# Optimization experiments

Measured on AMD Instinct MI355X. Metric: run time of the kernel, lower is better.

## Reference

```python
import jax, jax.numpy as jnp
import numpy as np

N = 100000
E = 1600000
DIM_IN, DIM_H, DIM_OUT = 48, 48, 48


def gcn_conv(x, edge_index, W, b):
    # PyG GCNConv: add self-loops, symmetric normalization D^-1/2 (A+I) D^-1/2, linear first.
    n = x.shape[0]
    loop = jnp.arange(n, dtype=edge_index.dtype)
    row = jnp.concatenate([edge_index[0], loop])  # sources
    col = jnp.concatenate([edge_index[1], loop])  # targets
    deg = jax.ops.segment_sum(jnp.ones_like(col, dtype=x.dtype), col, num_segments=n)
    dinv = jnp.where(deg > 0, jax.lax.rsqrt(jnp.maximum(deg, 1e-12)), 0.0)
    norm = dinv[row] * dinv[col]  # [E+N]
    h = x @ W  # [N, out]
    msg = h[row] * norm[:, None]  # gather + scale, [E+N, out]
    out = jax.ops.segment_sum(msg, col, num_segments=n)  # scatter-add
    return out + b


def setup_inputs() -> dict:
    key = jax.random.key(0)
    ks = jax.random.split(key, 8)
    x = jax.random.normal(ks[0], (N, DIM_IN), dtype=jnp.float32)
    edge_index = jax.random.randint(ks[1], (2, E), 0, N, dtype=jnp.int64)
    s1 = 1.0 / np.sqrt(DIM_IN)
    s2 = 1.0 / np.sqrt(DIM_H)
    s3 = 1.0 / np.sqrt(DIM_OUT)
    W1 = jax.random.uniform(ks[2], (DIM_IN, DIM_H), jnp.float32, -s1, s1)
    b1 = jnp.zeros((DIM_H,), jnp.float32)
    W2 = jax.random.uniform(ks[3], (DIM_H, DIM_OUT), jnp.float32, -s2, s2)
    b2 = jnp.zeros((DIM_OUT,), jnp.float32)
    Wlin = jax.random.uniform(ks[4], (DIM_OUT, 2), jnp.float32, -s3, s3)
    blin = jax.random.uniform(ks[5], (2,), jnp.float32, -s3, s3)
    return {"x": x, "edge_index": edge_index, "W1": W1, "b1": b1, "W2": W2, "b2": b2, "Wlin": Wlin, "blin": blin}


def reference(x, edge_index, W1, b1, W2, b2, Wlin, blin):
    h = gcn_conv(x, edge_index, W1, b1)
    h = jax.nn.leaky_relu(h, negative_slope=0.01)
    h = gcn_conv(h, edge_index, W2, b2)
    # global_add_pool with all-zero batch ids -> sum over all nodes, [1, DIM_OUT]
    g = jnp.sum(h, axis=0, keepdims=True)
    # dropout is identity in eval mode
    return g @ Wlin + blin  # [1, 2]
```

## Files before the change

### kernel.cpp

```cpp
#include <hip/hip_runtime.h>
#include <hip/hip_bf16.h>
#include <hip/hip_fp8.h>

#define DIM 48
#define HS8 48
#define BKN 256
#define BSH 8
#define CAP 5248
#define NB1MAX 400
#define EPT 12
#define GNPB 64
#define GTPN 3

typedef float v2f __attribute__((ext_vector_type(2)));

__device__ inline unsigned pack_fp8x4(float a, float b, float c, float d) {
#if __has_builtin(__builtin_amdgcn_cvt_pk_fp8_f32)
    int w = __builtin_amdgcn_cvt_pk_fp8_f32(a, b, 0, false);
    w = __builtin_amdgcn_cvt_pk_fp8_f32(c, d, w, true);
    return (unsigned)w;
#else
    __hip_fp8_e4m3 qa(a), qb(b), qc(c), qd(d);
    return (unsigned)qa.__x | ((unsigned)qb.__x << 8) |
           ((unsigned)qc.__x << 16) | ((unsigned)qd.__x << 24);
#endif
}

__device__ inline void acc_fp8x4(unsigned w, float* acc) {
#if __has_builtin(__builtin_amdgcn_cvt_pk_f32_fp8)
    v2f lo = __builtin_amdgcn_cvt_pk_f32_fp8((int)w, false);
    v2f hi = __builtin_amdgcn_cvt_pk_f32_fp8((int)w, true);
    acc[0] += lo[0]; acc[1] += lo[1]; acc[2] += hi[0]; acc[3] += hi[1];
#else
    __hip_fp8_e4m3 q0, q1, q2, q3;
    q0.__x = (unsigned char)(w & 0xff);
    q1.__x = (unsigned char)((w >> 8) & 0xff);
    q2.__x = (unsigned char)((w >> 16) & 0xff);
    q3.__x = (unsigned char)(w >> 24);
    acc[0] += (float)q0; acc[1] += (float)q1;
    acc[2] += (float)q2; acc[3] += (float)q3;
#endif
}

__device__ inline void acc_fp8x16(uint4 v, float* acc) {
    acc_fp8x4(v.x, acc + 0);
    acc_fp8x4(v.y, acc + 4);
    acc_fp8x4(v.z, acc + 8);
    acc_fp8x4(v.w, acc + 12);
}

__global__ void k_zero(int* __restrict__ cntc, int* __restrict__ cntr,
                       float* __restrict__ g, int nb1) {
    int i = blockIdx.x * blockDim.x + threadIdx.x;
    if (i < nb1) { cntc[i] = 0; cntr[i] = 0; }
    if (i < 64) g[i] = 0.0f;
}

__global__ __launch_bounds__(256) void k_part(
    const int* __restrict__ row, const int* __restrict__ col,
    int* __restrict__ cntc, int* __restrict__ cntr,
    unsigned* __restrict__ partc, unsigned* __restrict__ partr, int E, int nb1) {
    __shared__ int hc[NB1MAX], hr[NB1MAX];
    __shared__ int bc_[NB1MAX], br_[NB1MAX];
    int t = threadIdx.x;
    int lo = blockIdx.x * (256 * EPT);
    int hi = min(lo + 256 * EPT, E);
    int ec[EPT], er[EPT];
    int m = 0;
    for (int e = lo + t; e < hi; e += 256) { ec[m] = col[e]; er[m] = row[e]; ++m; }
    for (int i = t; i < nb1; i += 256) { hc[i] = 0; hr[i] = 0; }
    __syncthreads();
    for (int k = 0; k < m; ++k) {
        atomicAdd(&hc[ec[k] >> BSH], 1);
        atomicAdd(&hr[er[k] >> BSH], 1);
    }
    __syncthreads();
    for (int i = t; i < nb1; i += 256) {
        bc_[i] = hc[i] ? atomicAdd(&cntc[i], hc[i]) : 0;
        br_[i] = hr[i] ? atomicAdd(&cntr[i], hr[i]) : 0;
        hc[i] = 0; hr[i] = 0;
    }
    __syncthreads();
    for (int k = 0; k < m; ++k) {
        int c = ec[k], r = er[k];
        int b1 = c >> BSH;
        unsigned p1 = (unsigned)(bc_[b1] + atomicAdd(&hc[b1], 1));
        if (p1 < (unsigned)CAP)
            partc[(size_t)b1 * CAP + p1] = ((unsigned)(c & (BKN - 1)) << 24) | (unsigned)r;
        int b2 = r >> BSH;
        unsigned p2 = (unsigned)(br_[b2] + atomicAdd(&hr[b2], 1));
        if (p2 < (unsigned)CAP)
            partr[(size_t)b2 * CAP + p2] = ((unsigned)(r & (BKN - 1)) << 24) | (unsigned)c;
    }
}

__global__ __launch_bounds__(256) void k_sortp(
    const unsigned* __restrict__ partc, const int* __restrict__ cntc,
    int* __restrict__ nodpk, float* __restrict__ dinv,
    int* __restrict__ srcs, int N, int nb1) {
    __shared__ int cnt[BKN];
    __shared__ int cur[BKN];
    __shared__ int sc[256];
    __shared__ int outb[CAP];
    int b = blockIdx.x, t = threadIdx.x;
    int nlo = b << BSH;
    int nE = min(cntc[b], CAP);
    const unsigned* pp = partc + (size_t)b * CAP;
    cnt[t] = 0;
    __syncthreads();
    for (int e = t; e < nE; e += 256)
        atomicAdd(&cnt[pp[e] >> 24], 1);
    __syncthreads();
    int v = cnt[t];
    sc[t] = v;
    __syncthreads();
    for (int off = 1; off < 256; off <<= 1) {
        int u = (t >= off) ? sc[t - off] : 0;
        __syncthreads();
        sc[t] += u;
        __syncthreads();
    }
    int ex = (t == 0) ? 0 : sc[t - 1];
    if (nlo + t < N) {
        nodpk[nlo + t] = ex | (v << 16);
        dinv[nlo + t] = 1.0f / sqrtf((float)(v + 1));
    }
    cur[t] = ex;
    __syncthreads();
    for (int e = t; e < nE; e += 256) {
        unsigned p = pp[e];
        int s = atomicAdd(&cur[p >> 24], 1);
        outb[s] = (int)(p & 0xffffffu);
    }
    __syncthreads();
    int* sb = srcs + (size_t)b * CAP;
    for (int i2 = t; i2 < nE; i2 += 256) sb[i2] = outb[i2];
}

__global__ __launch_bounds__(256) void k_wsum(
    const unsigned* __restrict__ partr, const int* __restrict__ cntr,
    const float* __restrict__ dinv, float* __restrict__ wfin, int N, int nb1) {
    __shared__ float ws[BKN];
    int b = blockIdx.x, t = threadIdx.x;
    ws[t] = 0.0f;
    __syncthreads();
    int nE = min(cntr[b], CAP);
    const unsigned* pp = partr + (size_t)b * CAP;
    for (int e = t; e < nE; e += 256) {
        unsigned p = pp[e];
        atomicAdd(&ws[p >> 24], dinv[p & 0xffffffu]);
    }
    __syncthreads();
    int j = (b << BSH) + t;
    if (j < N) {
        float dj = dinv[j];
        wfin[j] = (ws[t] + dj) * dj;
    }
}

__global__ void k_mm_scale(const float* __restrict__ in, const float* __restrict__ W,
                           const float* __restrict__ dinv,
                           unsigned char* __restrict__ hs8, int n) {
    __shared__ float Ws[DIM * DIM];
    for (int i = threadIdx.x; i < DIM * DIM; i += blockDim.x) Ws[i] = W[i];
    __syncthreads();
    int node = blockIdx.x * blockDim.x + threadIdx.x;
    if (node >= n) return;
    float xr[DIM];
    const float4* xp = (const float4*)(in + (size_t)node * DIM);
    #pragma unroll
    for (int j = 0; j < DIM / 4; ++j) {
        float4 v = xp[j];
        xr[j * 4 + 0] = v.x; xr[j * 4 + 1] = v.y;
        xr[j * 4 + 2] = v.z; xr[j * 4 + 3] = v.w;
    }
    float o[DIM];
    #pragma unroll
    for (int f = 0; f < DIM; ++f) o[f] = 0.0f;
    for (int k = 0; k < DIM; ++k) {
        float xv = xr[k];
        #pragma unroll
        for (int f = 0; f < DIM; ++f) o[f] = fmaf(xv, Ws[k * DIM + f], o[f]);
    }
    float d = dinv[node];
    uint4* hp = (uint4*)(hs8 + (size_t)node * HS8);
    #pragma unroll
    for (int q = 0; q < 3; ++q) {
        uint4 v;
        v.x = pack_fp8x4(o[q*16+ 0]*d, o[q*16+ 1]*d, o[q*16+ 2]*d, o[q*16+ 3]*d);
        v.y = pack_fp8x4(o[q*16+ 4]*d, o[q*16+ 5]*d, o[q*16+ 6]*d, o[q*16+ 7]*d);
        v.z = pack_fp8x4(o[q*16+ 8]*d, o[q*16+ 9]*d, o[q*16+10]*d, o[q*16+11]*d);
        v.w = pack_fp8x4(o[q*16+12]*d, o[q*16+13]*d, o[q*16+14]*d, o[q*16+15]*d);
        hp[q] = v;
    }
}

__global__ __launch_bounds__(GNPB * GTPN) void k_gather1f(
    const unsigned char* __restrict__ hs8,
    const int* __restrict__ nodpk, const int* __restrict__ srcs,
    const float* __restrict__ dinv, const float* __restrict__ wfin,
    const float* __restrict__ bias, float* __restrict__ g, int n) {
    __shared__ float gsum[DIM];
    int t = threadIdx.x;
    if (t < DIM) gsum[t] = 0.0f;
    __syncthreads();
    int local = t / GTPN;
    int c = t - local * GTPN;
    int i = blockIdx.x * GNPB + local;
    bool valid = (i < n);
    float ov[16];
    if (valid) {
        int pk = nodpk[i];
        int start = (i >> BSH) * CAP + (pk & 0xffff);
        int end = start + (pk >> 16);
        float d = dinv[i];
        float w = wfin[i];
        const unsigned char* hb = hs8 + (size_t)c * 16;
        float acc[16];
        #pragma unroll
        for (int k = 0; k < 16; ++k) acc[k] = 0.0f;
        uint4 sv = *(const uint4*)(hb + (size_t)i * HS8);
        acc_fp8x16(sv, acc);
        for (int j = start; j < end; ++j) {
            uint4 v = *(const uint4*)(hb + (size_t)srcs[j] * HS8);
            acc_fp8x16(v, acc);
        }
        #pragma unroll
        for (int k = 0; k < 16; ++k) {
            float vv = acc[k] * d + bias[c * 16 + k];
            vv = (vv >= 0.0f) ? vv : 0.01f * vv;
            ov[k] = vv * w;
        }
    }
    if (valid) {
        #pragma unroll
        for (int k = 0; k < 16; ++k) atomicAdd(&gsum[c * 16 + k], ov[k]);
    }
    __syncthreads();
    if (t < DIM) atomicAdd(&g[t], gsum[t]);
}

__global__ void k_final2(const float* __restrict__ g, const float* __restrict__ W2,
                         const float* __restrict__ b2, const float* __restrict__ Wlin,
                         const float* __restrict__ blin, float* __restrict__ out, int n) {
    __shared__ float gp[DIM];
    int t = threadIdx.x;
    if (t < DIM) {
        float s = (float)n * b2[t];
        for (int q = 0; q < DIM; ++q) s += g[q] * W2[q * DIM + t];
        gp[t] = s;
    }
    __syncthreads();
    if (t < 2) {
        float s = blin[t];
        for (int f = 0; f < DIM; ++f) s += gp[f] * Wlin[f * 2 + t];
        out[t] = s;
    }
}

static inline char* alignup(char* p, size_t a) {
    return (char*)(((uintptr_t)p + a - 1) & ~(uintptr_t)(a - 1));
}

extern "C" void kernel_launch(void* const* d_in, const int* in_sizes, int n_in,
                              void* d_out, int out_size, void* d_ws, size_t ws_size,
                              hipStream_t stream) {
    const float* x    = (const float*)d_in[0];
    const int*   ei   = (const int*)d_in[1];
    const float* W1   = (const float*)d_in[2];
    const float* b1   = (const float*)d_in[3];
    const float* W2   = (const float*)d_in[4];
    const float* b2   = (const float*)d_in[5];
    const float* Wlin = (const float*)d_in[6];
    const float* blin = (const float*)d_in[7];
    float* out = (float*)d_out;

    int N = in_sizes[0] / DIM;
    int E = in_sizes[1] / 2;
    const int* row = ei;
    const int* col = ei + E;
    int nb1 = (N + BKN - 1) / BKN;

    char* p = (char*)d_ws;
    int* cntc = (int*)p;                  p = alignup(p + nb1 * 4, 64);
    int* cntr = (int*)p;                  p = alignup(p + nb1 * 4, 64);
    int* nodpk = (int*)p;                 p = alignup(p + (size_t)N * 4, 64);
    float* dinv = (float*)p;              p = alignup(p + (size_t)N * 4, 64);
    float* wfin = (float*)p;              p = alignup(p + (size_t)N * 4, 64);
    float* g = (float*)p;                 p = alignup(p + 64 * 4, 64);
    unsigned* partc = (unsigned*)p;       p = alignup(p + (size_t)nb1 * CAP * 4, 64);
    unsigned* partr = (unsigned*)p;       p = alignup(p + (size_t)nb1 * CAP * 4, 64);
    int* srcs = (int*)p;                  p = alignup(p + (size_t)nb1 * CAP * 4, 64);
    unsigned char* hs8 = (unsigned char*)p;

    int nblk = (N + 255) / 256;
    int gblk = (N + GNPB - 1) / GNPB;
    int pblk = (E + 256 * EPT - 1) / (256 * EPT);

    k_zero<<<(nb1 + 255) / 256, 256, 0, stream>>>(cntc, cntr, g, nb1);
    k_part<<<pblk, 256, 0, stream>>>(row, col, cntc, cntr, partc, partr, E, nb1);
    k_sortp<<<nb1, 256, 0, stream>>>(partc, cntc, nodpk, dinv, srcs, N, nb1);
    k_wsum<<<nb1, 256, 0, stream>>>(partr, cntr, dinv, wfin, N, nb1);

    k_mm_scale<<<nblk, 256, 0, stream>>>(x, W1, dinv, hs8, N);
    k_gather1f<<<gblk, GNPB * GTPN, 0, stream>>>(hs8, nodpk, srcs, dinv, wfin, b1, g, N);

    k_final2<<<1, 64, 0, stream>>>(g, W2, b2, Wlin, blin, out, N);
}
```

Baseline: 158.4 us.

## Split fp8 feature table into three planar slices and gather each in separate pass

The fp8 node feature table is stored as three separate 16-byte-per-node arrays, and the aggregation runs as three launches, one per 16-feature slice. Each pass gathers from a smaller array, which should fit better in cache for the random neighbour reads. Two threads per node split the neighbour list with four loads in flight each and combine by shuffle. In exchange, edge indices and per-node metadata are re-read three times and there are two extra kernel launches.

```diff
diff --git a/kernel.cpp b/kernel.cpp
--- a/kernel.cpp
+++ b/kernel.cpp
@@ -3,14 +3,11 @@
 #include <hip/hip_fp8.h>
 
 #define DIM 48
-#define HS8 48
 #define BKN 256
 #define BSH 8
 #define CAP 5248
 #define NB1MAX 400
 #define EPT 12
-#define GNPB 64
-#define GTPN 3
 
 typedef float v2f __attribute__((ext_vector_type(2)));
 
@@ -160,7 +157,9 @@
 
 __global__ void k_mm_scale(const float* __restrict__ in, const float* __restrict__ W,
                            const float* __restrict__ dinv,
-                           unsigned char* __restrict__ hs8, int n) {
+                           unsigned char* __restrict__ hsA,
+                           unsigned char* __restrict__ hsB,
+                           unsigned char* __restrict__ hsC, int n) {
     __shared__ float Ws[DIM * DIM];
     for (int i = threadIdx.x; i < DIM * DIM; i += blockDim.x) Ws[i] = W[i];
     __syncthreads();
@@ -183,61 +182,81 @@
         for (int f = 0; f < DIM; ++f) o[f] = fmaf(xv, Ws[k * DIM + f], o[f]);
     }
     float d = dinv[node];
-    uint4* hp = (uint4*)(hs8 + (size_t)node * HS8);
-    #pragma unroll
-    for (int q = 0; q < 3; ++q) {
-        uint4 v;
-        v.x = pack_fp8x4(o[q*16+ 0]*d, o[q*16+ 1]*d, o[q*16+ 2]*d, o[q*16+ 3]*d);
-        v.y = pack_fp8x4(o[q*16+ 4]*d, o[q*16+ 5]*d, o[q*16+ 6]*d, o[q*16+ 7]*d);
-        v.z = pack_fp8x4(o[q*16+ 8]*d, o[q*16+ 9]*d, o[q*16+10]*d, o[q*16+11]*d);
-        v.w = pack_fp8x4(o[q*16+12]*d, o[q*16+13]*d, o[q*16+14]*d, o[q*16+15]*d);
-        hp[q] = v;
-    }
-}
-
-__global__ __launch_bounds__(GNPB * GTPN) void k_gather1f(
-    const unsigned char* __restrict__ hs8,
+    #pragma unroll
+    for (int f = 0; f < DIM; ++f) o[f] *= d;
+    uint4 v;
+    v.x = pack_fp8x4(o[0], o[1], o[2], o[3]);
+    v.y = pack_fp8x4(o[4], o[5], o[6], o[7]);
+    v.z = pack_fp8x4(o[8], o[9], o[10], o[11]);
+    v.w = pack_fp8x4(o[12], o[13], o[14], o[15]);
+    *(uint4*)(hsA + (size_t)node * 16) = v;
+    v.x = pack_fp8x4(o[16], o[17], o[18], o[19]);
+    v.y = pack_fp8x4(o[20], o[21], o[22], o[23]);
+    v.z = pack_fp8x4(o[24], o[25], o[26], o[27]);
+    v.w = pack_fp8x4(o[28], o[29], o[30], o[31]);
+    *(uint4*)(hsB + (size_t)node * 16) = v;
+    v.x = pack_fp8x4(o[32], o[33], o[34], o[35]);
+    v.y = pack_fp8x4(o[36], o[37], o[38], o[39]);
+    v.z = pack_fp8x4(o[40], o[41], o[42], o[43]);
+    v.w = pack_fp8x4(o[44], o[45], o[46], o[47]);
+    *(uint4*)(hsC + (size_t)node * 16) = v;
+}
+
+template <int Q>
+__global__ __launch_bounds__(256) void k_gather3(
+    const unsigned char* __restrict__ hsq,
     const int* __restrict__ nodpk, const int* __restrict__ srcs,
     const float* __restrict__ dinv, const float* __restrict__ wfin,
     const float* __restrict__ bias, float* __restrict__ g, int n) {
-    __shared__ float gsum[DIM];
+    __shared__ float gsum[16];
     int t = threadIdx.x;
-    if (t < DIM) gsum[t] = 0.0f;
-    __syncthreads();
-    int local = t / GTPN;
-    int c = t - local * GTPN;
-    int i = blockIdx.x * GNPB + local;
+    if (t < 16) gsum[t] = 0.0f;
+    __syncthreads();
+    int local = t >> 1;
+    int p = t & 1;
+    int i = blockIdx.x * 128 + local;
     bool valid = (i < n);
-    float ov[16];
+    float acc[16];
+    #pragma unroll
+    for (int k = 0; k < 16; ++k) acc[k] = 0.0f;
+    float d = 0.0f, w = 0.0f;
     if (valid) {
         int pk = nodpk[i];
         int start = (i >> BSH) * CAP + (pk & 0xffff);
-        int end = start + (pk >> 16);
-        float d = dinv[i];
-        float w = wfin[i];
-        const unsigned char* hb = hs8 + (size_t)c * 16;
-        float acc[16];
-        #pragma unroll
-        for (int k = 0; k < 16; ++k) acc[k] = 0.0f;
-        uint4 sv = *(const uint4*)(hb + (size_t)i * HS8);
-        acc_fp8x16(sv, acc);
-        for (int j = start; j < end; ++j) {
-            uint4 v = *(const uint4*)(hb + (size_t)srcs[j] * HS8);
+        int nv = (pk >> 16) + 1;
+        d = dinv[i];
+        w = wfin[i];
+        int kv = p;
+        for (; kv + 6 < nv; kv += 8) {
+            int s0 = (kv == 0) ? i : srcs[start + kv - 1];
+            int s1 = srcs[start + kv + 1];
+            int s2 = srcs[start + kv + 3];
+            int s3 = srcs[start + kv + 5];
+            uint4 v0 = *(const uint4*)(hsq + (size_t)s0 * 16);
+            uint4 v1 = *(const uint4*)(hsq + (size_t)s1 * 16);
+            uint4 v2 = *(const uint4*)(hsq + (size_t)s2 * 16);
+            uint4 v3 = *(const uint4*)(hsq + (size_t)s3 * 16);
+            acc_fp8x16(v0, acc); acc_fp8x16(v1, acc);
+            acc_fp8x16(v2, acc); acc_fp8x16(v3, acc);
+        }
+        for (; kv < nv; kv += 2) {
+            int s = (kv == 0) ? i : srcs[start + kv - 1];
+            uint4 v = *(const uint4*)(hsq + (size_t)s * 16);
             acc_fp8x16(v, acc);
         }
+    }
+    #pragma unroll
+    for (int k = 0; k < 16; ++k) acc[k] += __shfl_xor(acc[k], 1);
+    if (valid && p == 0) {
         #pragma unroll
         for (int k = 0; k < 16; ++k) {
-            float vv = acc[k] * d + bias[c * 16 + k];
+            float vv = acc[k] * d + bias[Q * 16 + k];
             vv = (vv >= 0.0f) ? vv : 0.01f * vv;
-            ov[k] = vv * w;
+            atomicAdd(&gsum[k], vv * w);
         }
     }
-    if (valid) {
-        #pragma unroll
-        for (int k = 0; k < 16; ++k) atomicAdd(&gsum[c * 16 + k], ov[k]);
-    }
-    __syncthreads();
-    if (t < DIM) atomicAdd(&g[t], gsum[t]);
+    __syncthreads();
+    if (t < 16) atomicAdd(&g[Q * 16 + t], gsum[t]);
 }
 
 __global__ void k_final2(const float* __restrict__ g, const float* __restrict__ W2,
@@ -291,10 +310,12 @@
     unsigned* partc = (unsigned*)p;       p = alignup(p + (size_t)nb1 * CAP * 4, 64);
     unsigned* partr = (unsigned*)p;       p = alignup(p + (size_t)nb1 * CAP * 4, 64);
     int* srcs = (int*)p;                  p = alignup(p + (size_t)nb1 * CAP * 4, 64);
-    unsigned char* hs8 = (unsigned char*)p;
+    unsigned char* hsA = (unsigned char*)p; p = alignup(p + (size_t)N * 16, 64);
+    unsigned char* hsB = (unsigned char*)p; p = alignup(p + (size_t)N * 16, 64);
+    unsigned char* hsC = (unsigned char*)p;
 
     int nblk = (N + 255) / 256;
-    int gblk = (N + GNPB - 1) / GNPB;
+    int gblk = (N + 127) / 128;
     int pblk = (E + 256 * EPT - 1) / (256 * EPT);
 
     k_zero<<<(nb1 + 255) / 256, 256, 0, stream>>>(cntc, cntr, g, nb1);
@@ -302,8 +323,11 @@
     k_sortp<<<nb1, 256, 0, stream>>>(partc, cntc, nodpk, dinv, srcs, N, nb1);
     k_wsum<<<nb1, 256, 0, stream>>>(partr, cntr, dinv, wfin, N, nb1);
 
-    k_mm_scale<<<nblk, 256, 0, stream>>>(x, W1, dinv, hs8, N);
-    k_gather1f<<<gblk, GNPB * GTPN, 0, stream>>>(hs8, nodpk, srcs, dinv, wfin, b1, g, N);
+    k_mm_scale<<<nblk, 256, 0, stream>>>(x, W1, dinv, hsA, hsB, hsC, N);
+
+    k_gather3<0><<<gblk, 256, 0, stream>>>(hsA, nodpk, srcs, dinv, wfin, b1, g, N);
+    k_gather3<1><<<gblk, 256, 0, stream>>>(hsB, nodpk, srcs, dinv, wfin, b1, g, N);
+    k_gather3<2><<<gblk, 256, 0, stream>>>(hsC, nodpk, srcs, dinv, wfin, b1, g, N);
 
     k_final2<<<1, 64, 0, stream>>>(g, W2, b2, Wlin, blin, out, N);
 }
```

After: 210.2 us. 1.33x slower.
